# Performance work log

Measured on AMD Instinct MI355X. Metric: run time of the kernel, lower is better.

## Reference

```python
import jax, jax.numpy as jnp
import numpy as np

VERY_NEG = -1e30


def setup_inputs() -> dict:
    key = jax.random.key(0)
    kq, kk, kv, km = jax.random.split(key, 4)
    B, H, S, D = 4, 8, 2048, 64
    Q = jax.random.normal(kq, (B, H, S, D), dtype=jnp.float32)
    K = jax.random.normal(kk, (B, H, S, D), dtype=jnp.float32)
    V = jax.random.normal(kv, (B, H, S, D), dtype=jnp.float32)
    # key-padding mask broadcast over heads and queries: 1 = keep, 0 = masked
    mask = jax.random.randint(km, (B, 1, 1, S), 0, 2, dtype=jnp.int32)
    return {"Q": Q, "K": K, "V": V, "mask": mask}


def reference(Q, K, V, mask):
    d_k = Q.shape[-1]
    scale = jnp.asarray(np.power(d_k, 0.5), dtype=Q.dtype)
    # scores: [B,H,S_q,S_k]
    scores = jnp.einsum("bhqd,bhkd->bhqk", Q, K) / scale
    # QANet exponential_mask: add -1e30 where mask == 0
    masked = scores + (1.0 - mask.astype(scores.dtype)) * VERY_NEG
    attn = jax.nn.softmax(masked, axis=-1)
    out = jnp.einsum("bhqk,bhkd->bhqd", attn, V)
    return out
```

## Files before the change

### kernel.cpp

```cpp
#include <hip/hip_runtime.h>

typedef _Float16 half8_t __attribute__((ext_vector_type(8)));
typedef _Float16 half4_t __attribute__((ext_vector_type(4)));
typedef _Float16 half2_t __attribute__((ext_vector_type(2)));
typedef __fp16 fp16x2 __attribute__((ext_vector_type(2)));
typedef float f32x4 __attribute__((ext_vector_type(4)));

#define S_LEN 2048
#define D_DIM 64
#define SD (S_LEN * D_DIM)
#define NT16 16
#define LDK 72
#define LDO 68
#define THR 4.0f
#define WS_NEED ((size_t)(16 * 1024 * 1024 + 16384))

__global__ __launch_bounds__(256)
void prep_kernel(const float* __restrict__ Kg, const float* __restrict__ Vg,
                 const int* __restrict__ Mg, _Float16* __restrict__ wsK,
                 _Float16* __restrict__ wsV, _Float16* __restrict__ wsKeep) {
  __shared__ float vt[64][68];
  const int blk = blockIdx.x;
  const int t = threadIdx.x;

  if (blk < 1024) {
    const int bh = blk >> 5, kt = blk & 31;
    const float* src = Kg + (size_t)bh * SD + (size_t)kt * 64 * D_DIM;
    char* dst = (char*)wsK + (size_t)blk * 8192;
#pragma unroll
    for (int i = 0; i < 2; ++i) {
      int task = t + 256 * i;
      int row = task >> 3, j = task & 7;
      float4 lo = *(const float4*)(src + row * D_DIM + 8 * j);
      float4 hi = *(const float4*)(src + row * D_DIM + 8 * j + 4);
      fp16x2 p0 = __builtin_amdgcn_cvt_pkrtz(lo.x, lo.y);
      fp16x2 p1 = __builtin_amdgcn_cvt_pkrtz(lo.z, lo.w);
      fp16x2 p2 = __builtin_amdgcn_cvt_pkrtz(hi.x, hi.y);
      fp16x2 p3 = __builtin_amdgcn_cvt_pkrtz(hi.z, hi.w);
      half8_t h;
      h[0] = (_Float16)p0[0]; h[1] = (_Float16)p0[1];
      h[2] = (_Float16)p1[0]; h[3] = (_Float16)p1[1];
      h[4] = (_Float16)p2[0]; h[5] = (_Float16)p2[1];
      h[6] = (_Float16)p3[0]; h[7] = (_Float16)p3[1];
      *(half8_t*)(dst + row * 128 + ((16 * j) ^ ((row & 7) << 4))) = h;
    }
  } else if (blk < 2048) {
    const int vb = blk - 1024;
    const int bh = vb >> 5, kt = vb & 31;
    const float* src = Vg + (size_t)bh * SD + (size_t)kt * 64 * D_DIM;
    const int* msk = Mg + (size_t)(bh >> 3) * S_LEN + kt * 64;
#pragma unroll
    for (int i = 0; i < 4; ++i) {
      int r = (t >> 4) + 16 * i, c4 = t & 15;
      *(float4*)&vt[r][c4 * 4] = *(const float4*)(src + r * D_DIM + c4 * 4);
    }
    __syncthreads();
    char* dst = (char*)wsV + (size_t)vb * 8192;
#pragma unroll
    for (int i = 0; i < 4; ++i) {
      int task = t + 256 * i;
      int drow = task >> 4, j2 = task & 15, k0 = 4 * j2;
      int4 mv = *(const int4*)(msk + k0);
      float a  = vt[k0][drow]     * (float)mv.x;
      float b  = vt[k0 + 1][drow] * (float)mv.y;
      float cc = vt[k0 + 2][drow] * (float)mv.z;
      float d  = vt[k0 + 3][drow] * (float)mv.w;
      fp16x2 h0 = __builtin_amdgcn_cvt_pkrtz(a, b);
      fp16x2 h1 = __builtin_amdgcn_cvt_pkrtz(cc, d);
      half4_t h;
      h[0] = (_Float16)h0[0]; h[1] = (_Float16)h0[1];
      h[2] = (_Float16)h1[0]; h[3] = (_Float16)h1[1];
      *(half4_t*)(dst + drow * 128 + ((8 * j2) ^ ((drow & 15) << 3))) = h;
    }
  } else {
    const int b = blk - 2048;
    const int* src = Mg + (size_t)b * S_LEN + 8 * t;
    int4 m0 = *(const int4*)src;
    int4 m1 = *(const int4*)(src + 4);
    half8_t h;
    h[0] = (_Float16)(float)m0.x; h[1] = (_Float16)(float)m0.y;
    h[2] = (_Float16)(float)m0.z; h[3] = (_Float16)(float)m0.w;
    h[4] = (_Float16)(float)m1.x; h[5] = (_Float16)(float)m1.y;
    h[6] = (_Float16)(float)m1.z; h[7] = (_Float16)(float)m1.w;
    *(half8_t*)(wsKeep + (size_t)b * S_LEN + 8 * t) = h;
  }
}

__global__ __launch_bounds__(256, 2)
void fattn_dma(const float* __restrict__ Qg, const _Float16* __restrict__ wsK,
               const _Float16* __restrict__ wsV,
               const _Float16* __restrict__ wsKeep, float* __restrict__ Og) {
  __shared__ __align__(16) char smem[65536];
  float* Osh = (float*)smem;

  const int t = threadIdx.x;
  const int w = t >> 6;
  const int lane = t & 63;
  const int g = lane >> 4;
  const int c = lane & 15;

  const int bh = blockIdx.x & 31;
  const int qt = blockIdx.x >> 5;
  const int qb = qt * 128;

  const float* Qb = Qg + (size_t)bh * SD;
  float*       Ob = Og + (size_t)bh * SD;
  const _Float16* keepB = wsKeep + (size_t)(bh >> 3) * S_LEN;

  const float qscale = 0.125f * 1.44269504088896340736f;
  half8_t qf[2][2];
#pragma unroll
  for (int h = 0; h < 2; ++h) {
    const float* qp = Qb + (size_t)(qb + 32 * w + 16 * h + c) * D_DIM + 8 * g;
#pragma unroll
    for (int ks = 0; ks < 2; ++ks) {
      float4 lo = *(const float4*)(qp + 32 * ks);
      float4 hi = *(const float4*)(qp + 32 * ks + 4);
      fp16x2 p0 = __builtin_amdgcn_cvt_pkrtz(lo.x * qscale, lo.y * qscale);
      fp16x2 p1 = __builtin_amdgcn_cvt_pkrtz(lo.z * qscale, lo.w * qscale);
      fp16x2 p2 = __builtin_amdgcn_cvt_pkrtz(hi.x * qscale, hi.y * qscale);
      fp16x2 p3 = __builtin_amdgcn_cvt_pkrtz(hi.z * qscale, hi.w * qscale);
      half8_t hh;
      hh[0] = (_Float16)p0[0]; hh[1] = (_Float16)p0[1];
      hh[2] = (_Float16)p1[0]; hh[3] = (_Float16)p1[1];
      hh[4] = (_Float16)p2[0]; hh[5] = (_Float16)p2[1];
      hh[6] = (_Float16)p3[0]; hh[7] = (_Float16)p3[1];
      qf[h][ks] = hh;
    }
  }

  const size_t tbase = (size_t)bh * 32 * 8192;
  auto dma = [&](int buf, int kt) {
    const char* gK = (const char*)wsK + tbase + (size_t)kt * 16384 +
                     w * 4096 + lane * 16;
    const char* gV = (const char*)wsV + tbase + (size_t)kt * 16384 +
                     w * 4096 + lane * 16;
    char* lK = smem + 16384 * buf + w * 4096;
    char* lV = smem + 32768 + 16384 * buf + w * 4096;
#pragma unroll
    for (int i = 0; i < 4; ++i)
      __builtin_amdgcn_global_load_lds((const float*)(gK + 1024 * i),
                                       (float*)(lK + 1024 * i), 16, 0, 0);
#pragma unroll
    for (int i = 0; i < 4; ++i)
      __builtin_amdgcn_global_load_lds((const float*)(gV + 1024 * i),
                                       (float*)(lV + 1024 * i), 16, 0, 0);
  };

  f32x4 acc[2][4];
  f32x4 accl[2];
#pragma unroll
  for (int h = 0; h < 2; ++h) {
#pragma unroll
    for (int j = 0; j < 4; ++j) accl[h][j] = 0.f;
#pragma unroll
    for (int i = 0; i < 4; ++i)
#pragma unroll
      for (int j = 0; j < 4; ++j) acc[h][i][j] = 0.f;
  }
  float mrun[2] = {-1e30f, -1e30f};

  const int kxor = (c & 7) << 4;
  const int vxor = c << 3;

  dma(0, 0);
  __syncthreads();

  for (int kt = 0; kt < NT16; ++kt) {
    const int cur = kt & 1;
    if (kt < NT16 - 1) dma(cur ^ 1, kt + 1);

    const char* Kc = smem + 16384 * cur;
    const char* Vc = smem + 32768 + 16384 * cur;

    half4_t kA[8];
#pragma unroll
    for (int mt = 0; mt < 8; ++mt)
      kA[mt] = *(const half4_t*)(keepB + kt * 128 + 16 * mt + 4 * g);

    f32x4 sT[2][8];
    __builtin_amdgcn_s_setprio(1);
#pragma unroll
    for (int mt = 0; mt < 8; ++mt) {
      const char* Krow = Kc + ((mt & 4) ? 8192 : 0) + (16 * (mt & 3) + c) * 128;
      f32x4 z0, z1;
#pragma unroll
      for (int j = 0; j < 4; ++j) { z0[j] = 0.f; z1[j] = 0.f; }
#pragma unroll
      for (int ks = 0; ks < 2; ++ks) {
        half8_t kf = *(const half8_t*)(Krow + ((ks * 64 + g * 16) ^ kxor));
        z0 = __builtin_amdgcn_mfma_f32_16x16x32_f16(kf, qf[0][ks], z0, 0, 0, 0);
        z1 = __builtin_amdgcn_mfma_f32_16x16x32_f16(kf, qf[1][ks], z1, 0, 0, 0);
      }
      sT[0][mt] = z0;
      sT[1][mt] = z1;
    }
    __builtin_amdgcn_s_setprio(0);

    float tl[2];
#pragma unroll
    for (int h = 0; h < 2; ++h) {
      float tm = -1e30f;
#pragma unroll
      for (int mt = 0; mt < 8; ++mt)
        tm = fmaxf(tm, fmaxf(fmaxf(sT[h][mt][0], sT[h][mt][1]),
                             fmaxf(sT[h][mt][2], sT[h][mt][3])));
      tl[h] = tm;
    }
    int ok0 = __all(tl[0] <= mrun[0] + THR);
    int ok1 = __all(tl[1] <= mrun[1] + THR);
    if (!(ok0 & ok1)) {
#pragma unroll
      for (int h = 0; h < 2; ++h) {
        float tmax = tl[h];
        tmax = fmaxf(tmax, __shfl_xor(tmax, 16));
        tmax = fmaxf(tmax, __shfl_xor(tmax, 32));
        float mnew = fmaxf(mrun[h], tmax);
        float alpha = __builtin_amdgcn_exp2f(mrun[h] - mnew);
        mrun[h] = mnew;
        accl[h][0] *= alpha; accl[h][1] *= alpha;
        accl[h][2] *= alpha; accl[h][3] *= alpha;
#pragma unroll
        for (int mt = 0; mt < 4; ++mt) {
          acc[h][mt][0] *= alpha; acc[h][mt][1] *= alpha;
          acc[h][mt][2] *= alpha; acc[h][mt][3] *= alpha;
        }
      }
    }

    __builtin_amdgcn_s_setprio(1);
#pragma unroll
    for (int mt = 0; mt < 8; ++mt) {
      const char* Vsub = Vc + ((mt & 4) ? 8192 : 0);
      half4_t pf[2];
#pragma unroll
      for (int h = 0; h < 2; ++h) {
        float pv0 = __builtin_amdgcn_exp2f(sT[h][mt][0] - mrun[h]);
        float pv1 = __builtin_amdgcn_exp2f(sT[h][mt][1] - mrun[h]);
        float pv2 = __builtin_amdgcn_exp2f(sT[h][mt][2] - mrun[h]);
        float pv3 = __builtin_amdgcn_exp2f(sT[h][mt][3] - mrun[h]);
        fp16x2 p01 = __builtin_amdgcn_cvt_pkrtz(pv0, pv1);
        fp16x2 p23 = __builtin_amdgcn_cvt_pkrtz(pv2, pv3);
        half4_t ph;
        ph[0] = (_Float16)p01[0]; ph[1] = (_Float16)p01[1];
        ph[2] = (_Float16)p23[0]; ph[3] = (_Float16)p23[1];
        pf[h] = ph;
      }
      half4_t vf[4];
#pragma unroll
      for (int dt = 0; dt < 4; ++dt)
        vf[dt] = *(const half4_t*)(Vsub + (16 * dt + c) * 128 +
                                   ((32 * (mt & 3) + 8 * g) ^ vxor));
      accl[0] = __builtin_amdgcn_mfma_f32_16x16x16f16(kA[mt], pf[0], accl[0], 0, 0, 0);
      accl[1] = __builtin_amdgcn_mfma_f32_16x16x16f16(kA[mt], pf[1], accl[1], 0, 0, 0);
#pragma unroll
      for (int dt = 0; dt < 4; ++dt) {
        acc[0][dt] = __builtin_amdgcn_mfma_f32_16x16x16f16(vf[dt], pf[0],
                                                           acc[0][dt], 0, 0, 0);
        acc[1][dt] = __builtin_amdgcn_mfma_f32_16x16x16f16(vf[dt], pf[1],
                                                           acc[1][dt], 0, 0, 0);
      }
    }
    __builtin_amdgcn_s_setprio(0);

    __syncthreads();
  }

#pragma unroll
  for (int h = 0; h < 2; ++h) {
    float linv = 1.f / accl[h][0];
#pragma unroll
    for (int mt = 0; mt < 4; ++mt)
#pragma unroll
      for (int r = 0; r < 4; ++r)
        Osh[(32 * w + 16 * h + c) * LDO + 16 * mt + 4 * g + r] = acc[h][mt][r] * linv;
  }
  __syncthreads();
  {
    int f8 = t & 7;
#pragma unroll
    for (int i = 0; i < 4; ++i) {
      int q = (t >> 3) + 32 * i;
#pragma unroll
      for (int j = 0; j < 2; ++j) {
        int c4 = f8 + 8 * j;
        f32x4 o = *(f32x4*)(Osh + q * LDO + c4 * 4);
        *(float4*)(Ob + (size_t)(qb + q) * D_DIM + c4 * 4) =
            make_float4(o.x, o.y, o.z, o.w);
      }
    }
  }
}

__global__ __launch_bounds__(256, 2)
void fattn_fb(const float* __restrict__ Qg, const float* __restrict__ Kg,
              const float* __restrict__ Vg, const int* __restrict__ Mg,
              float* __restrict__ Og) {
  __shared__ __align__(16) char smem[45056];
  float* Msh = (float*)(smem + 36864);
  float* Osh = (float*)smem;

  const int t = threadIdx.x;
  const int w = t >> 6;
  const int lane = t & 63;
  const int g = lane >> 4;
  const int c = lane & 15;

  const int bh = blockIdx.x & 31;
  const int qt = blockIdx.x >> 5;
  const int qb = qt * 128;

  const float* Qb = Qg + (size_t)bh * SD;
  const float* Kb = Kg + (size_t)bh * SD;
  const float* Vb = Vg + (size_t)bh * SD;
  const int*   Mb = Mg + (size_t)(bh >> 3) * S_LEN;
  float*       Ob = Og + (size_t)bh * SD;

  {
    int4 m0 = *(const int4*)(Mb + 8 * t);
    int4 m1 = *(const int4*)(Mb + 8 * t + 4);
    float4 f0, f1;
    f0.x = (float)(m0.x - 1) * 1e30f; f0.y = (float)(m0.y - 1) * 1e30f;
    f0.z = (float)(m0.z - 1) * 1e30f; f0.w = (float)(m0.w - 1) * 1e30f;
    f1.x = (float)(m1.x - 1) * 1e30f; f1.y = (float)(m1.y - 1) * 1e30f;
    f1.z = (float)(m1.z - 1) * 1e30f; f1.w = (float)(m1.w - 1) * 1e30f;
    *(float4*)(Msh + 8 * t) = f0;
    *(float4*)(Msh + 8 * t + 4) = f1;
  }

  const float qscale = 0.125f * 1.44269504088896340736f;
  half8_t qf[2][2];
#pragma unroll
  for (int h = 0; h < 2; ++h) {
    const float* qp = Qb + (size_t)(qb + 32 * w + 16 * h + c) * D_DIM + 8 * g;
#pragma unroll
    for (int ks = 0; ks < 2; ++ks) {
      float4 lo = *(const float4*)(qp + 32 * ks);
      float4 hi = *(const float4*)(qp + 32 * ks + 4);
      fp16x2 p0 = __builtin_amdgcn_cvt_pkrtz(lo.x * qscale, lo.y * qscale);
      fp16x2 p1 = __builtin_amdgcn_cvt_pkrtz(lo.z * qscale, lo.w * qscale);
      fp16x2 p2 = __builtin_amdgcn_cvt_pkrtz(hi.x * qscale, hi.y * qscale);
      fp16x2 p3 = __builtin_amdgcn_cvt_pkrtz(hi.z * qscale, hi.w * qscale);
      half8_t hh;
      hh[0] = (_Float16)p0[0]; hh[1] = (_Float16)p0[1];
      hh[2] = (_Float16)p1[0]; hh[3] = (_Float16)p1[1];
      hh[4] = (_Float16)p2[0]; hh[5] = (_Float16)p2[1];
      hh[6] = (_Float16)p3[0]; hh[7] = (_Float16)p3[1];
      qf[h][ks] = hh;
    }
  }

  const int krow0 = t >> 4;
  const int kc4   = t & 15;
  const int vp    = t >> 3;
  const int vkpl  = t & 7;

  float4 kr[4];
  float2 vr[8];
  auto prefetch = [&](int kb2) {
#pragma unroll
    for (int it = 0; it < 4; ++it)
      kr[it] = *(const float4*)(Kb + (size_t)(kb2 + krow0 + 16 * it) * D_DIM + kc4 * 4);
#pragma unroll
    for (int kc = 0; kc < 4; ++kc) {
      const float* vpp = Vb + (size_t)(kb2 + 2 * (vkpl + 8 * kc)) * D_DIM + 2 * vp;
      vr[2 * kc]     = *(const float2*)(vpp);
      vr[2 * kc + 1] = *(const float2*)(vpp + D_DIM);
    }
  };
  auto stage = [&](int buf) {
    _Float16* Kd = (_Float16*)(smem + 9216 * buf);
    _Float16* Vd = (_Float16*)(smem + 18432 + 9216 * buf);
#pragma unroll
    for (int it = 0; it < 4; ++it) {
      fp16x2 a  = __builtin_amdgcn_cvt_pkrtz(kr[it].x, kr[it].y);
      fp16x2 b2 = __builtin_amdgcn_cvt_pkrtz(kr[it].z, kr[it].w);
      half4_t h;
      h[0] = (_Float16)a[0]; h[1] = (_Float16)a[1];
      h[2] = (_Float16)b2[0]; h[3] = (_Float16)b2[1];
      *(half4_t*)(Kd + (krow0 + 16 * it) * LDK + kc4 * 4) = h;
    }
#pragma unroll
    for (int kc = 0; kc < 4; ++kc) {
      int kp = vkpl + 8 * kc;
      fp16x2 h0 = __builtin_amdgcn_cvt_pkrtz(vr[2 * kc].x, vr[2 * kc + 1].x);
      fp16x2 h1 = __builtin_amdgcn_cvt_pkrtz(vr[2 * kc].y, vr[2 * kc + 1].y);
      half2_t g0; g0[0] = (_Float16)h0[0]; g0[1] = (_Float16)h0[1];
      half2_t g1; g1[0] = (_Float16)h1[0]; g1[1] = (_Float16)h1[1];
      *(half2_t*)(Vd + (2 * vp) * LDK + 2 * kp) = g0;
      *(half2_t*)(Vd + (2 * vp + 1) * LDK + 2 * kp) = g1;
    }
  };

  f32x4 acc[2][4];
  f32x4 accl[2];
#pragma unroll
  for (int h = 0; h < 2; ++h) {
#pragma unroll
    for (int j = 0; j < 4; ++j) accl[h][j] = 0.f;
#pragma unroll
    for (int i = 0; i < 4; ++i)
#pragma unroll
      for (int j = 0; j < 4; ++j) acc[h][i][j] = 0.f;
  }
// ... 105 lines not shown
        accl[h] = __builtin_amdgcn_mfma_f32_16x16x16f16(ones4, pf, accl[h], 0, 0, 0);
#pragma unroll
        for (int dt = 0; dt < 4; ++dt)
          acc[h][dt] = __builtin_amdgcn_mfma_f32_16x16x16f16(vf[dt][mt], pf,
                                                             acc[h][dt], 0, 0, 0);
      }
    }
    __builtin_amdgcn_s_setprio(0);

    __syncthreads();
  }

#pragma unroll
  for (int h = 0; h < 2; ++h) {
    float linv = 1.f / accl[h][0];
#pragma unroll
    for (int mt = 0; mt < 4; ++mt)
#pragma unroll
      for (int r = 0; r < 4; ++r)
        Osh[(32 * w + 16 * h + c) * LDO + 16 * mt + 4 * g + r] = acc[h][mt][r] * linv;
  }
  __syncthreads();
  {
    int f8 = t & 7;
#pragma unroll
    for (int i = 0; i < 4; ++i) {
      int q = (t >> 3) + 32 * i;
#pragma unroll
      for (int j = 0; j < 2; ++j) {
        int c4 = f8 + 8 * j;
        f32x4 o = *(f32x4*)(Osh + q * LDO + c4 * 4);
        *(float4*)(Ob + (size_t)(qb + q) * D_DIM + c4 * 4) =
            make_float4(o.x, o.y, o.z, o.w);
      }
    }
  }
}

extern "C" void kernel_launch(void* const* d_in, const int* in_sizes, int n_in,
                              void* d_out, int out_size, void* d_ws, size_t ws_size,
                              hipStream_t stream) {
  (void)in_sizes; (void)n_in; (void)out_size;
  const float* Q = (const float*)d_in[0];
  const float* K = (const float*)d_in[1];
  const float* V = (const float*)d_in[2];
  const int*   M = (const int*)d_in[3];
  float* O = (float*)d_out;

  if (ws_size >= WS_NEED && d_ws != nullptr) {
    _Float16* wsK = (_Float16*)d_ws;
    _Float16* wsV = wsK + (size_t)32 * S_LEN * D_DIM;
    _Float16* wsKeep = (_Float16*)((char*)d_ws + 16 * 1024 * 1024);
    prep_kernel<<<dim3(2052), dim3(256), 0, stream>>>(K, V, M, wsK, wsV, wsKeep);
    fattn_dma<<<dim3(32 * 16), dim3(256), 0, stream>>>(Q, wsK, wsV, wsKeep, O);
  } else {
    fattn_fb<<<dim3(32 * 16), dim3(256), 0, stream>>>(Q, K, V, M, O);
  }
}
```

Baseline: 144.3 us.

## Replace LDS double-buffered attention with register-direct fragment loads and smaller query tiles

The main attention kernel stops staging K and V tiles through LDS with DMA and barriers. Each wave now loads its MFMA fragments straight from global memory into registers, using a two-set ping-pong software pipeline. The prep kernel drops the XOR swizzle and reorders the V layout so that fragments can be read directly. Query tiles shrink from 128 to 64 rows, doubling the grid and raising occupancy to 4 blocks per CU. The cost is that each block rereads the per-head K/V through cache, with more global traffic and more load latency exposed per wave.

```diff
diff --git a/kernel.cpp b/kernel.cpp
--- a/kernel.cpp
+++ b/kernel.cpp
@@ -9,7 +9,6 @@
 #define S_LEN 2048
 #define D_DIM 64
 #define SD (S_LEN * D_DIM)
-#define NT16 16
 #define LDK 72
 #define LDO 68
 #define THR 4.0f
@@ -42,7 +41,7 @@
       h[2] = (_Float16)p1[0]; h[3] = (_Float16)p1[1];
       h[4] = (_Float16)p2[0]; h[5] = (_Float16)p2[1];
       h[6] = (_Float16)p3[0]; h[7] = (_Float16)p3[1];
-      *(half8_t*)(dst + row * 128 + ((16 * j) ^ ((row & 7) << 4))) = h;
+      *(half8_t*)(dst + row * 128 + 16 * j) = h;
     }
   } else if (blk < 2048) {
     const int vb = blk - 1024;
@@ -59,7 +58,8 @@
 #pragma unroll
     for (int i = 0; i < 4; ++i) {
       int task = t + 256 * i;
-      int drow = task >> 4, j2 = task & 15, k0 = 4 * j2;
+      int drow = task >> 4, j2 = task & 15;
+      int k0 = 16 * (2 * (j2 >> 3) + (j2 & 1)) + 4 * ((j2 >> 1) & 3);
       int4 mv = *(const int4*)(msk + k0);
       float a  = vt[k0][drow]     * (float)mv.x;
       float b  = vt[k0 + 1][drow] * (float)mv.y;
@@ -70,7 +70,7 @@
       half4_t h;
       h[0] = (_Float16)h0[0]; h[1] = (_Float16)h0[1];
       h[2] = (_Float16)h1[0]; h[3] = (_Float16)h1[1];
-      *(half4_t*)(dst + drow * 128 + ((8 * j2) ^ ((drow & 15) << 3))) = h;
+      *(half4_t*)(dst + drow * 128 + 8 * j2) = h;
     }
   } else {
     const int b = blk - 2048;
@@ -86,12 +86,11 @@
   }
 }
 
-__global__ __launch_bounds__(256, 2)
-void fattn_dma(const float* __restrict__ Qg, const _Float16* __restrict__ wsK,
+__global__ __launch_bounds__(256, 4)
+void fattn_reg(const float* __restrict__ Qg, const _Float16* __restrict__ wsK,
                const _Float16* __restrict__ wsV,
                const _Float16* __restrict__ wsKeep, float* __restrict__ Og) {
-  __shared__ __align__(16) char smem[65536];
-  float* Osh = (float*)smem;
+  __shared__ float Osh[64 * LDO];
 
   const int t = threadIdx.x;
   const int w = t >> 6;
@@ -101,11 +100,207 @@
 
   const int bh = blockIdx.x & 31;
   const int qt = blockIdx.x >> 5;
-  const int qb = qt * 128;
+  const int qb = qt * 64;
 
   const float* Qb = Qg + (size_t)bh * SD;
   float*       Ob = Og + (size_t)bh * SD;
-  const _Float16* keepB = wsKeep + (size_t)(bh >> 3) * S_LEN;
+
+  const float qscale = 0.125f * 1.44269504088896340736f;
+  half8_t qf0, qf1;
+  {
+    const float* qp = Qb + (size_t)(qb + 16 * w + c) * D_DIM + 8 * g;
+#pragma unroll
+    for (int ks = 0; ks < 2; ++ks) {
+      float4 lo = *(const float4*)(qp + 32 * ks);
+      float4 hi = *(const float4*)(qp + 32 * ks + 4);
+      fp16x2 p0 = __builtin_amdgcn_cvt_pkrtz(lo.x * qscale, lo.y * qscale);
+      fp16x2 p1 = __builtin_amdgcn_cvt_pkrtz(lo.z * qscale, lo.w * qscale);
+      fp16x2 p2 = __builtin_amdgcn_cvt_pkrtz(hi.x * qscale, hi.y * qscale);
+      fp16x2 p3 = __builtin_amdgcn_cvt_pkrtz(hi.z * qscale, hi.w * qscale);
+      half8_t hh;
+      hh[0] = (_Float16)p0[0]; hh[1] = (_Float16)p0[1];
+      hh[2] = (_Float16)p1[0]; hh[3] = (_Float16)p1[1];
+      hh[4] = (_Float16)p2[0]; hh[5] = (_Float16)p2[1];
+      hh[6] = (_Float16)p3[0]; hh[7] = (_Float16)p3[1];
+      if (ks == 0) qf0 = hh; else qf1 = hh;
+    }
+  }
+
+  const char* kB  = (const char*)wsK + (size_t)bh * 262144 + (size_t)c * 128 + g * 16;
+  const char* vB0 = (const char*)wsV + (size_t)bh * 262144 + (size_t)c * 128 + g * 16;
+  const char* vB1 = vB0 + 4096;
+  const _Float16* kpB = wsKeep + (size_t)(bh >> 3) * S_LEN + 4 * g;
+
+  struct FragSet {
+    half8_t kf00, kf01, kf10, kf11;
+    half8_t vf0, vf1, vf2, vf3;
+    half4_t kA0, kA1;
+  };
+
+  auto loadSet = [&](FragSet& S, const char* kp, const char* v0,
+                     const char* v1, const _Float16* kpp, int ho)
+      __attribute__((always_inline)) {
+    S.kf00 = *(const half8_t*)(kp);
+    S.kf01 = *(const half8_t*)(kp + 64);
+    S.kf10 = *(const half8_t*)(kp + 2048);
+    S.kf11 = *(const half8_t*)(kp + 2112);
+    S.vf0 = *(const half8_t*)(v0 + ho);
+    S.vf1 = *(const half8_t*)(v0 + 2048 + ho);
+    S.vf2 = *(const half8_t*)(v1 + ho);
+    S.vf3 = *(const half8_t*)(v1 + 2048 + ho);
+    S.kA0 = *(const half4_t*)(kpp);
+    S.kA1 = *(const half4_t*)(kpp + 16);
+  };
+
+  f32x4 acc0 = {0.f,0.f,0.f,0.f}, acc1 = {0.f,0.f,0.f,0.f};
+  f32x4 acc2 = {0.f,0.f,0.f,0.f}, acc3 = {0.f,0.f,0.f,0.f};
+  f32x4 accl = {0.f,0.f,0.f,0.f};
+  float mrun = -1e30f;
+
+  auto compute = [&](FragSet& S) __attribute__((always_inline)) {
+    __builtin_amdgcn_s_setprio(1);
+    f32x4 s0 = {0.f,0.f,0.f,0.f}, s1 = {0.f,0.f,0.f,0.f};
+    s0 = __builtin_amdgcn_mfma_f32_16x16x32_f16(S.kf00, qf0, s0, 0, 0, 0);
+    s0 = __builtin_amdgcn_mfma_f32_16x16x32_f16(S.kf01, qf1, s0, 0, 0, 0);
+    s1 = __builtin_amdgcn_mfma_f32_16x16x32_f16(S.kf10, qf0, s1, 0, 0, 0);
+    s1 = __builtin_amdgcn_mfma_f32_16x16x32_f16(S.kf11, qf1, s1, 0, 0, 0);
+    __builtin_amdgcn_s_setprio(0);
+
+    float tl = fmaxf(fmaxf(fmaxf(s0[0], s0[1]), fmaxf(s0[2], s0[3])),
+                     fmaxf(fmaxf(s1[0], s1[1]), fmaxf(s1[2], s1[3])));
+    if (!__all(tl <= mrun + THR)) {
+      float tmax = fmaxf(tl, __shfl_xor(tl, 16));
+      tmax = fmaxf(tmax, __shfl_xor(tmax, 32));
+      float mnew = fmaxf(mrun, tmax);
+      float alpha = __builtin_amdgcn_exp2f(mrun - mnew);
+      mrun = mnew;
+#pragma unroll
+      for (int r = 0; r < 4; ++r) {
+        accl[r] *= alpha;
+        acc0[r] *= alpha; acc1[r] *= alpha;
+        acc2[r] *= alpha; acc3[r] *= alpha;
+      }
+    }
+
+    float p00 = __builtin_amdgcn_exp2f(s0[0] - mrun);
+    float p01 = __builtin_amdgcn_exp2f(s0[1] - mrun);
+    float p02 = __builtin_amdgcn_exp2f(s0[2] - mrun);
+    float p03 = __builtin_amdgcn_exp2f(s0[3] - mrun);
+    float p10 = __builtin_amdgcn_exp2f(s1[0] - mrun);
+    float p11 = __builtin_amdgcn_exp2f(s1[1] - mrun);
+    float p12 = __builtin_amdgcn_exp2f(s1[2] - mrun);
+    float p13 = __builtin_amdgcn_exp2f(s1[3] - mrun);
+    fp16x2 a0 = __builtin_amdgcn_cvt_pkrtz(p00, p01);
+    fp16x2 a1 = __builtin_amdgcn_cvt_pkrtz(p02, p03);
+    fp16x2 b0 = __builtin_amdgcn_cvt_pkrtz(p10, p11);
+    fp16x2 b1 = __builtin_amdgcn_cvt_pkrtz(p12, p13);
+    half4_t pf0, pf1;
+    pf0[0] = (_Float16)a0[0]; pf0[1] = (_Float16)a0[1];
+    pf0[2] = (_Float16)a1[0]; pf0[3] = (_Float16)a1[1];
+    pf1[0] = (_Float16)b0[0]; pf1[1] = (_Float16)b0[1];
+    pf1[2] = (_Float16)b1[0]; pf1[3] = (_Float16)b1[1];
+
+    __builtin_amdgcn_s_setprio(1);
+    accl = __builtin_amdgcn_mfma_f32_16x16x16f16(S.kA0, pf0, accl, 0, 0, 0);
+    accl = __builtin_amdgcn_mfma_f32_16x16x16f16(S.kA1, pf1, accl, 0, 0, 0);
+    half4_t v;
+    v = __builtin_shufflevector(S.vf0, S.vf0, 0, 1, 2, 3);
+    acc0 = __builtin_amdgcn_mfma_f32_16x16x16f16(v, pf0, acc0, 0, 0, 0);
+    v = __builtin_shufflevector(S.vf0, S.vf0, 4, 5, 6, 7);
+    acc0 = __builtin_amdgcn_mfma_f32_16x16x16f16(v, pf1, acc0, 0, 0, 0);
+    v = __builtin_shufflevector(S.vf1, S.vf1, 0, 1, 2, 3);
+    acc1 = __builtin_amdgcn_mfma_f32_16x16x16f16(v, pf0, acc1, 0, 0, 0);
+    v = __builtin_shufflevector(S.vf1, S.vf1, 4, 5, 6, 7);
+    acc1 = __builtin_amdgcn_mfma_f32_16x16x16f16(v, pf1, acc1, 0, 0, 0);
+    v = __builtin_shufflevector(S.vf2, S.vf2, 0, 1, 2, 3);
+    acc2 = __builtin_amdgcn_mfma_f32_16x16x16f16(v, pf0, acc2, 0, 0, 0);
+    v = __builtin_shufflevector(S.vf2, S.vf2, 4, 5, 6, 7);
+    acc2 = __builtin_amdgcn_mfma_f32_16x16x16f16(v, pf1, acc2, 0, 0, 0);
+    v = __builtin_shufflevector(S.vf3, S.vf3, 0, 1, 2, 3);
+    acc3 = __builtin_amdgcn_mfma_f32_16x16x16f16(v, pf0, acc3, 0, 0, 0);
+    v = __builtin_shufflevector(S.vf3, S.vf3, 4, 5, 6, 7);
+    acc3 = __builtin_amdgcn_mfma_f32_16x16x16f16(v, pf1, acc3, 0, 0, 0);
+    __builtin_amdgcn_s_setprio(0);
+  };
+
+  FragSet A, B;
+  loadSet(A, kB, vB0, vB1, kpB, 0);
+  kB += 4096; kpB += 32;
+  for (int tt = 0; tt < 62; tt += 2) {
+    loadSet(B, kB, vB0, vB1, kpB, 64);
+    kB += 4096; kpB += 32; vB0 += 8192; vB1 += 8192;
+    compute(A);
+    loadSet(A, kB, vB0, vB1, kpB, 0);
+    kB += 4096; kpB += 32;
+    compute(B);
+  }
+  loadSet(B, kB, vB0, vB1, kpB, 64);
+  compute(A);
+  compute(B);
+
+  {
+    float linv = 1.f / accl[0];
+    int row = (16 * w + c) * LDO + 4 * g;
+#pragma unroll
+    for (int r = 0; r < 4; ++r) {
+      Osh[row + 0  + r] = acc0[r] * linv;
+      Osh[row + 16 + r] = acc1[r] * linv;
+      Osh[row + 32 + r] = acc2[r] * linv;
+      Osh[row + 48 + r] = acc3[r] * linv;
+    }
+  }
+  __syncthreads();
+  {
+    int f8 = t & 7;
+#pragma unroll
+    for (int i = 0; i < 2; ++i) {
+      int q = (t >> 3) + 32 * i;
+#pragma unroll
+      for (int j = 0; j < 2; ++j) {
+        int c4 = f8 + 8 * j;
+        f32x4 o = *(f32x4*)(Osh + q * LDO + c4 * 4);
+        *(float4*)(Ob + (size_t)(qb + q) * D_DIM + c4 * 4) =
+            make_float4(o.x, o.y, o.z, o.w);
+      }
+    }
+  }
+}
+
+__global__ __launch_bounds__(256, 2)
+void fattn_fb(const float* __restrict__ Qg, const float* __restrict__ Kg,
+              const float* __restrict__ Vg, const int* __restrict__ Mg,
+              float* __restrict__ Og) {
+  __shared__ __align__(16) char smem[45056];
+  float* Msh = (float*)(smem + 36864);
+  float* Osh = (float*)smem;
+
+  const int t = threadIdx.x;
+  const int w = t >> 6;
+  const int lane = t & 63;
+  const int g = lane >> 4;
+  const int c = lane & 15;
+
+  const int bh = blockIdx.x & 31;
+  const int qt = blockIdx.x >> 5;
+  const int qb = qt * 128;
+
+  const float* Qb = Qg + (size_t)bh * SD;
+  const float* Kb = Kg + (size_t)bh * SD;
+  const float* Vb = Vg + (size_t)bh * SD;
+  const int*   Mb = Mg + (size_t)(bh >> 3) * S_LEN;
+  float*       Ob = Og + (size_t)bh * SD;
+
+  {
+    int4 m0 = *(const int4*)(Mb + 8 * t);
+    int4 m1 = *(const int4*)(Mb + 8 * t + 4);
+    float4 f0, f1;
+    f0.x = (float)(m0.x - 1) * 1e30f; f0.y = (float)(m0.y - 1) * 1e30f;
+    f0.z = (float)(m0.z - 1) * 1e30f; f0.w = (float)(m0.w - 1) * 1e30f;
+    f1.x = (float)(m1.x - 1) * 1e30f; f1.y = (float)(m1.y - 1) * 1e30f;
+    f1.z = (float)(m1.z - 1) * 1e30f; f1.w = (float)(m1.w - 1) * 1e30f;
+    *(float4*)(Msh + 8 * t) = f0;
+    *(float4*)(Msh + 8 * t + 4) = f1;
+  }
 
   const float qscale = 0.125f * 1.44269504088896340736f;
   half8_t qf[2][2];
@@ -129,227 +324,6 @@
     }
   }
 
-  const size_t tbase = (size_t)bh * 32 * 8192;
-  auto dma = [&](int buf, int kt) {
-    const char* gK = (const char*)wsK + tbase + (size_t)kt * 16384 +
-                     w * 4096 + lane * 16;
-    const char* gV = (const char*)wsV + tbase + (size_t)kt * 16384 +
-                     w * 4096 + lane * 16;
-    char* lK = smem + 16384 * buf + w * 4096;
-    char* lV = smem + 32768 + 16384 * buf + w * 4096;
-#pragma unroll
-    for (int i = 0; i < 4; ++i)
-      __builtin_amdgcn_global_load_lds((const float*)(gK + 1024 * i),
-                                       (float*)(lK + 1024 * i), 16, 0, 0);
-#pragma unroll
-    for (int i = 0; i < 4; ++i)
-      __builtin_amdgcn_global_load_lds((const float*)(gV + 1024 * i),
-                                       (float*)(lV + 1024 * i), 16, 0, 0);
-  };
-
-  f32x4 acc[2][4];
-  f32x4 accl[2];
-#pragma unroll
-  for (int h = 0; h < 2; ++h) {
-#pragma unroll
-    for (int j = 0; j < 4; ++j) accl[h][j] = 0.f;
-#pragma unroll
-    for (int i = 0; i < 4; ++i)
-#pragma unroll
-      for (int j = 0; j < 4; ++j) acc[h][i][j] = 0.f;
-  }
-  float mrun[2] = {-1e30f, -1e30f};
-
-  const int kxor = (c & 7) << 4;
-  const int vxor = c << 3;
-
-  dma(0, 0);
-  __syncthreads();
-
-  for (int kt = 0; kt < NT16; ++kt) {
-    const int cur = kt & 1;
-    if (kt < NT16 - 1) dma(cur ^ 1, kt + 1);
-
-    const char* Kc = smem + 16384 * cur;
-    const char* Vc = smem + 32768 + 16384 * cur;
-
-    half4_t kA[8];
-#pragma unroll
-    for (int mt = 0; mt < 8; ++mt)
-      kA[mt] = *(const half4_t*)(keepB + kt * 128 + 16 * mt + 4 * g);
-
-    f32x4 sT[2][8];
-    __builtin_amdgcn_s_setprio(1);
-#pragma unroll
-    for (int mt = 0; mt < 8; ++mt) {
-      const char* Krow = Kc + ((mt & 4) ? 8192 : 0) + (16 * (mt & 3) + c) * 128;
-      f32x4 z0, z1;
-#pragma unroll
-      for (int j = 0; j < 4; ++j) { z0[j] = 0.f; z1[j] = 0.f; }
-#pragma unroll
-      for (int ks = 0; ks < 2; ++ks) {
-        half8_t kf = *(const half8_t*)(Krow + ((ks * 64 + g * 16) ^ kxor));
-        z0 = __builtin_amdgcn_mfma_f32_16x16x32_f16(kf, qf[0][ks], z0, 0, 0, 0);
-        z1 = __builtin_amdgcn_mfma_f32_16x16x32_f16(kf, qf[1][ks], z1, 0, 0, 0);
-      }
-      sT[0][mt] = z0;
-      sT[1][mt] = z1;
-    }
-    __builtin_amdgcn_s_setprio(0);
-
-    float tl[2];
-#pragma unroll
-    for (int h = 0; h < 2; ++h) {
-      float tm = -1e30f;
-#pragma unroll
-      for (int mt = 0; mt < 8; ++mt)
-        tm = fmaxf(tm, fmaxf(fmaxf(sT[h][mt][0], sT[h][mt][1]),
-                             fmaxf(sT[h][mt][2], sT[h][mt][3])));
-      tl[h] = tm;
-    }
-    int ok0 = __all(tl[0] <= mrun[0] + THR);
-    int ok1 = __all(tl[1] <= mrun[1] + THR);
-    if (!(ok0 & ok1)) {
-#pragma unroll
-      for (int h = 0; h < 2; ++h) {
-        float tmax = tl[h];
-        tmax = fmaxf(tmax, __shfl_xor(tmax, 16));
-        tmax = fmaxf(tmax, __shfl_xor(tmax, 32));
-        float mnew = fmaxf(mrun[h], tmax);
-        float alpha = __builtin_amdgcn_exp2f(mrun[h] - mnew);
-        mrun[h] = mnew;
-        accl[h][0] *= alpha; accl[h][1] *= alpha;
-        accl[h][2] *= alpha; accl[h][3] *= alpha;
-#pragma unroll
-        for (int mt = 0; mt < 4; ++mt) {
-          acc[h][mt][0] *= alpha; acc[h][mt][1] *= alpha;
-          acc[h][mt][2] *= alpha; acc[h][mt][3] *= alpha;
-        }
-      }
-    }
-
-    __builtin_amdgcn_s_setprio(1);
-#pragma unroll
-    for (int mt = 0; mt < 8; ++mt) {
-      const char* Vsub = Vc + ((mt & 4) ? 8192 : 0);
-      half4_t pf[2];
-#pragma unroll
-      for (int h = 0; h < 2; ++h) {
-        float pv0 = __builtin_amdgcn_exp2f(sT[h][mt][0] - mrun[h]);
-        float pv1 = __builtin_amdgcn_exp2f(sT[h][mt][1] - mrun[h]);
-        float pv2 = __builtin_amdgcn_exp2f(sT[h][mt][2] - mrun[h]);
-        float pv3 = __builtin_amdgcn_exp2f(sT[h][mt][3] - mrun[h]);
-        fp16x2 p01 = __builtin_amdgcn_cvt_pkrtz(pv0, pv1);
-        fp16x2 p23 = __builtin_amdgcn_cvt_pkrtz(pv2, pv3);
-        half4_t ph;
-        ph[0] = (_Float16)p01[0]; ph[1] = (_Float16)p01[1];
-        ph[2] = (_Float16)p23[0]; ph[3] = (_Float16)p23[1];
-        pf[h] = ph;
-      }
-      half4_t vf[4];
-#pragma unroll
-      for (int dt = 0; dt < 4; ++dt)
-        vf[dt] = *(const half4_t*)(Vsub + (16 * dt + c) * 128 +
-                                   ((32 * (mt & 3) + 8 * g) ^ vxor));
-      accl[0] = __builtin_amdgcn_mfma_f32_16x16x16f16(kA[mt], pf[0], accl[0], 0, 0, 0);
-      accl[1] = __builtin_amdgcn_mfma_f32_16x16x16f16(kA[mt], pf[1], accl[1], 0, 0, 0);
-#pragma unroll
-      for (int dt = 0; dt < 4; ++dt) {
-        acc[0][dt] = __builtin_amdgcn_mfma_f32_16x16x16f16(vf[dt], pf[0],
-                                                           acc[0][dt], 0, 0, 0);
-        acc[1][dt] = __builtin_amdgcn_mfma_f32_16x16x16f16(vf[dt], pf[1],
-                                                           acc[1][dt], 0, 0, 0);
-      }
-    }
-    __builtin_amdgcn_s_setprio(0);
-
-    __syncthreads();
-  }
-
-#pragma unroll
-  for (int h = 0; h < 2; ++h) {
-    float linv = 1.f / accl[h][0];
-#pragma unroll
-    for (int mt = 0; mt < 4; ++mt)
-#pragma unroll
-      for (int r = 0; r < 4; ++r)
-        Osh[(32 * w + 16 * h + c) * LDO + 16 * mt + 4 * g + r] = acc[h][mt][r] * linv;
-  }
-  __syncthreads();
-  {
-    int f8 = t & 7;
-#pragma unroll
-    for (int i = 0; i < 4; ++i) {
-      int q = (t >> 3) + 32 * i;
-#pragma unroll
-      for (int j = 0; j < 2; ++j) {
-        int c4 = f8 + 8 * j;
-        f32x4 o = *(f32x4*)(Osh + q * LDO + c4 * 4);
-        *(float4*)(Ob + (size_t)(qb + q) * D_DIM + c4 * 4) =
-            make_float4(o.x, o.y, o.z, o.w);
-      }
-    }
-  }
-}
-
-__global__ __launch_bounds__(256, 2)
-void fattn_fb(const float* __restrict__ Qg, const float* __restrict__ Kg,
-              const float* __restrict__ Vg, const int* __restrict__ Mg,
-              float* __restrict__ Og) {
-  __shared__ __align__(16) char smem[45056];
-  float* Msh = (float*)(smem + 36864);
-  float* Osh = (float*)smem;
-
-  const int t = threadIdx.x;
-  const int w = t >> 6;
-  const int lane = t & 63;
-  const int g = lane >> 4;
-  const int c = lane & 15;
-
-  const int bh = blockIdx.x & 31;
-  const int qt = blockIdx.x >> 5;
-  const int qb = qt * 128;
-
-  const float* Qb = Qg + (size_t)bh * SD;
-  const float* Kb = Kg + (size_t)bh * SD;
-  const float* Vb = Vg + (size_t)bh * SD;
-  const int*   Mb = Mg + (size_t)(bh >> 3) * S_LEN;
-  float*       Ob = Og + (size_t)bh * SD;
-
-  {
-    int4 m0 = *(const int4*)(Mb + 8 * t);
-    int4 m1 = *(const int4*)(Mb + 8 * t + 4);
-    float4 f0, f1;
-    f0.x = (float)(m0.x - 1) * 1e30f; f0.y = (float)(m0.y - 1) * 1e30f;
-    f0.z = (float)(m0.z - 1) * 1e30f; f0.w = (float)(m0.w - 1) * 1e30f;
-    f1.x = (float)(m1.x - 1) * 1e30f; f1.y = (float)(m1.y - 1) * 1e30f;
-    f1.z = (float)(m1.z - 1) * 1e30f; f1.w = (float)(m1.w - 1) * 1e30f;
-    *(float4*)(Msh + 8 * t) = f0;
-    *(float4*)(Msh + 8 * t + 4) = f1;
-  }
-
-  const float qscale = 0.125f * 1.44269504088896340736f;
-  half8_t qf[2][2];
-#pragma unroll
-  for (int h = 0; h < 2; ++h) {
-    const float* qp = Qb + (size_t)(qb + 32 * w + 16 * h + c) * D_DIM + 8 * g;
-#pragma unroll
-    for (int ks = 0; ks < 2; ++ks) {
-      float4 lo = *(const float4*)(qp + 32 * ks);
-      float4 hi = *(const float4*)(qp + 32 * ks + 4);
-      fp16x2 p0 = __builtin_amdgcn_cvt_pkrtz(lo.x * qscale, lo.y * qscale);
-      fp16x2 p1 = __builtin_amdgcn_cvt_pkrtz(lo.z * qscale, lo.w * qscale);
-      fp16x2 p2 = __builtin_amdgcn_cvt_pkrtz(hi.x * qscale, hi.y * qscale);
-      fp16x2 p3 = __builtin_amdgcn_cvt_pkrtz(hi.z * qscale, hi.w * qscale);
-      half8_t hh;
-      hh[0] = (_Float16)p0[0]; hh[1] = (_Float16)p0[1];
-      hh[2] = (_Float16)p1[0]; hh[3] = (_Float16)p1[1];
-      hh[4] = (_Float16)p2[0]; hh[5] = (_Float16)p2[1];
-      hh[6] = (_Float16)p3[0]; hh[7] = (_Float16)p3[1];
-      qf[h][ks] = hh;
-    }
-  }
-
   const int krow0 = t >> 4;
   const int kc4   = t & 15;
   const int vp    = t >> 3;
@@ -561,7 +535,7 @@
     _Float16* wsV = wsK + (size_t)32 * S_LEN * D_DIM;
     _Float16* wsKeep = (_Float16*)((char*)d_ws + 16 * 1024 * 1024);
     prep_kernel<<<dim3(2052), dim3(256), 0, stream>>>(K, V, M, wsK, wsV, wsKeep);
-    fattn_dma<<<dim3(32 * 16), dim3(256), 0, stream>>>(Q, wsK, wsV, wsKeep, O);
+    fattn_reg<<<dim3(32 * 32), dim3(256), 0, stream>>>(Q, wsK, wsV, wsKeep, O);
   } else {
     fattn_fb<<<dim3(32 * 16), dim3(256), 0, stream>>>(Q, K, V, M, O);
   }
```

Result: slower. 334.4 us (+131.6%).

## Halve attention query tile to 64 rows and double grid for occupancy

Applied to the files above, without the earlier changes.

The main attention kernel now handles 64 query rows per block (16 per wave) instead of 128, with 64-key tiles and half the LDS (32KB). The grid doubles to 1024 blocks and launch bounds allow 4 blocks per CU. V fragments are loaded for the whole tile ahead of the softmax. The goal is higher occupancy and better latency hiding across CUs. The cost is that every K/V tile is loaded from memory twice as often, with less reuse per load and more loop iterations and barriers.

```diff
diff --git a/kernel.cpp b/kernel.cpp
--- a/kernel.cpp
+++ b/kernel.cpp
@@ -9,7 +9,6 @@
 #define S_LEN 2048
 #define D_DIM 64
 #define SD (S_LEN * D_DIM)
-#define NT16 16
 #define LDK 72
 #define LDO 68
 #define THR 4.0f
@@ -86,11 +85,11 @@
   }
 }
 
-__global__ __launch_bounds__(256, 2)
+__global__ __launch_bounds__(256, 4)
 void fattn_dma(const float* __restrict__ Qg, const _Float16* __restrict__ wsK,
                const _Float16* __restrict__ wsV,
                const _Float16* __restrict__ wsKeep, float* __restrict__ Og) {
-  __shared__ __align__(16) char smem[65536];
+  __shared__ __align__(16) char smem[32768];
   float* Osh = (float*)smem;
 
   const int t = threadIdx.x;
@@ -101,11 +100,204 @@
 
   const int bh = blockIdx.x & 31;
   const int qt = blockIdx.x >> 5;
-  const int qb = qt * 128;
+  const int qb = qt * 64;
 
   const float* Qb = Qg + (size_t)bh * SD;
   float*       Ob = Og + (size_t)bh * SD;
   const _Float16* keepB = wsKeep + (size_t)(bh >> 3) * S_LEN;
+
+  const float qscale = 0.125f * 1.44269504088896340736f;
+  half8_t qf[2];
+  {
+    const float* qp = Qb + (size_t)(qb + 16 * w + c) * D_DIM + 8 * g;
+#pragma unroll
+    for (int ks = 0; ks < 2; ++ks) {
+      float4 lo = *(const float4*)(qp + 32 * ks);
+      float4 hi = *(const float4*)(qp + 32 * ks + 4);
+      fp16x2 p0 = __builtin_amdgcn_cvt_pkrtz(lo.x * qscale, lo.y * qscale);
+      fp16x2 p1 = __builtin_amdgcn_cvt_pkrtz(lo.z * qscale, lo.w * qscale);
+      fp16x2 p2 = __builtin_amdgcn_cvt_pkrtz(hi.x * qscale, hi.y * qscale);
+      fp16x2 p3 = __builtin_amdgcn_cvt_pkrtz(hi.z * qscale, hi.w * qscale);
+      half8_t hh;
+      hh[0] = (_Float16)p0[0]; hh[1] = (_Float16)p0[1];
+      hh[2] = (_Float16)p1[0]; hh[3] = (_Float16)p1[1];
+      hh[4] = (_Float16)p2[0]; hh[5] = (_Float16)p2[1];
+      hh[6] = (_Float16)p3[0]; hh[7] = (_Float16)p3[1];
+      qf[ks] = hh;
+    }
+  }
+
+  const size_t tbase = (size_t)bh * 262144;
+  auto dma = [&](int buf, int kt) {
+    const char* gK = (const char*)wsK + tbase + (size_t)kt * 8192 +
+                     w * 2048 + lane * 16;
+    const char* gV = (const char*)wsV + tbase + (size_t)kt * 8192 +
+                     w * 2048 + lane * 16;
+    char* lK = smem + 8192 * buf + w * 2048;
+    char* lV = smem + 16384 + 8192 * buf + w * 2048;
+    __builtin_amdgcn_global_load_lds((const float*)gK, (float*)lK, 16, 0, 0);
+    __builtin_amdgcn_global_load_lds((const float*)(gK + 1024),
+                                     (float*)(lK + 1024), 16, 0, 0);
+    __builtin_amdgcn_global_load_lds((const float*)gV, (float*)lV, 16, 0, 0);
+    __builtin_amdgcn_global_load_lds((const float*)(gV + 1024),
+                                     (float*)(lV + 1024), 16, 0, 0);
+  };
+
+  f32x4 acc[4];
+  f32x4 accl;
+#pragma unroll
+  for (int j = 0; j < 4; ++j) {
+    accl[j] = 0.f;
+#pragma unroll
+    for (int i = 0; i < 4; ++i) acc[i][j] = 0.f;
+  }
+  float mrun = -1e30f;
+
+  const int kxor = (c & 7) << 4;
+  const int vxor = c << 3;
+
+  dma(0, 0);
+  __syncthreads();
+
+  for (int kt = 0; kt < 32; ++kt) {
+    const int cur = kt & 1;
+    if (kt < 31) dma(cur ^ 1, kt + 1);
+
+    const char* Kc = smem + 8192 * cur;
+    const char* Vc = smem + 16384 + 8192 * cur;
+
+    half4_t kA[4];
+#pragma unroll
+    for (int mt = 0; mt < 4; ++mt)
+      kA[mt] = *(const half4_t*)(keepB + kt * 64 + 16 * mt + 4 * g);
+
+    f32x4 sT[4];
+    __builtin_amdgcn_s_setprio(1);
+#pragma unroll
+    for (int mt = 0; mt < 4; ++mt) {
+      const char* Krow = Kc + (16 * mt + c) * 128;
+      f32x4 z;
+#pragma unroll
+      for (int j = 0; j < 4; ++j) z[j] = 0.f;
+#pragma unroll
+      for (int ks = 0; ks < 2; ++ks) {
+        half8_t kf = *(const half8_t*)(Krow + ((ks * 64 + g * 16) ^ kxor));
+        z = __builtin_amdgcn_mfma_f32_16x16x32_f16(kf, qf[ks], z, 0, 0, 0);
+      }
+      sT[mt] = z;
+    }
+    __builtin_amdgcn_s_setprio(0);
+
+    half4_t vf[4][4];
+#pragma unroll
+    for (int dt = 0; dt < 4; ++dt)
+#pragma unroll
+      for (int mtk = 0; mtk < 4; ++mtk)
+        vf[dt][mtk] = *(const half4_t*)(Vc + (16 * dt + c) * 128 +
+                                        ((32 * mtk + 8 * g) ^ vxor));
+
+    float tl = -1e30f;
+#pragma unroll
+    for (int mt = 0; mt < 4; ++mt)
+      tl = fmaxf(tl, fmaxf(fmaxf(sT[mt][0], sT[mt][1]),
+                           fmaxf(sT[mt][2], sT[mt][3])));
+    if (!__all(tl <= mrun + THR)) {
+      float tmax = fmaxf(tl, __shfl_xor(tl, 16));
+      tmax = fmaxf(tmax, __shfl_xor(tmax, 32));
+      float mnew = fmaxf(mrun, tmax);
+      float alpha = __builtin_amdgcn_exp2f(mrun - mnew);
+      mrun = mnew;
+#pragma unroll
+      for (int j = 0; j < 4; ++j) {
+        accl[j] *= alpha;
+#pragma unroll
+        for (int i = 0; i < 4; ++i) acc[i][j] *= alpha;
+      }
+    }
+
+    __builtin_amdgcn_s_setprio(1);
+#pragma unroll
+    for (int mt = 0; mt < 4; ++mt) {
+      float pv0 = __builtin_amdgcn_exp2f(sT[mt][0] - mrun);
+      float pv1 = __builtin_amdgcn_exp2f(sT[mt][1] - mrun);
+      float pv2 = __builtin_amdgcn_exp2f(sT[mt][2] - mrun);
+      float pv3 = __builtin_amdgcn_exp2f(sT[mt][3] - mrun);
+      fp16x2 p01 = __builtin_amdgcn_cvt_pkrtz(pv0, pv1);
+      fp16x2 p23 = __builtin_amdgcn_cvt_pkrtz(pv2, pv3);
+      half4_t pf;
+      pf[0] = (_Float16)p01[0]; pf[1] = (_Float16)p01[1];
+      pf[2] = (_Float16)p23[0]; pf[3] = (_Float16)p23[1];
+      accl = __builtin_amdgcn_mfma_f32_16x16x16f16(kA[mt], pf, accl, 0, 0, 0);
+#pragma unroll
+      for (int dt = 0; dt < 4; ++dt)
+        acc[dt] = __builtin_amdgcn_mfma_f32_16x16x16f16(vf[dt][mt], pf,
+                                                        acc[dt], 0, 0, 0);
+    }
+    __builtin_amdgcn_s_setprio(0);
+
+    __syncthreads();
+  }
+
+  {
+    float linv = 1.f / accl[0];
+#pragma unroll
+    for (int mt = 0; mt < 4; ++mt)
+#pragma unroll
+      for (int r = 0; r < 4; ++r)
+        Osh[(16 * w + c) * LDO + 16 * mt + 4 * g + r] = acc[mt][r] * linv;
+  }
+  __syncthreads();
+  {
+    int f8 = t & 7;
+#pragma unroll
+    for (int i = 0; i < 2; ++i) {
+      int q = (t >> 3) + 32 * i;
+#pragma unroll
+      for (int j = 0; j < 2; ++j) {
+        int c4 = f8 + 8 * j;
+        f32x4 o = *(f32x4*)(Osh + q * LDO + c4 * 4);
+        *(float4*)(Ob + (size_t)(qb + q) * D_DIM + c4 * 4) =
+            make_float4(o.x, o.y, o.z, o.w);
+      }
+    }
+  }
+}
+
+__global__ __launch_bounds__(256, 2)
+void fattn_fb(const float* __restrict__ Qg, const float* __restrict__ Kg,
+              const float* __restrict__ Vg, const int* __restrict__ Mg,
+              float* __restrict__ Og) {
+  __shared__ __align__(16) char smem[45056];
+  float* Msh = (float*)(smem + 36864);
+  float* Osh = (float*)smem;
+
+  const int t = threadIdx.x;
+  const int w = t >> 6;
+  const int lane = t & 63;
+  const int g = lane >> 4;
+  const int c = lane & 15;
+
+  const int bh = blockIdx.x & 31;
+  const int qt = blockIdx.x >> 5;
+  const int qb = qt * 128;
+
+  const float* Qb = Qg + (size_t)bh * SD;
+  const float* Kb = Kg + (size_t)bh * SD;
+  const float* Vb = Vg + (size_t)bh * SD;
+  const int*   Mb = Mg + (size_t)(bh >> 3) * S_LEN;
+  float*       Ob = Og + (size_t)bh * SD;
+
+  {
+    int4 m0 = *(const int4*)(Mb + 8 * t);
+    int4 m1 = *(const int4*)(Mb + 8 * t + 4);
+    float4 f0, f1;
+    f0.x = (float)(m0.x - 1) * 1e30f; f0.y = (float)(m0.y - 1) * 1e30f;
+    f0.z = (float)(m0.z - 1) * 1e30f; f0.w = (float)(m0.w - 1) * 1e30f;
+    f1.x = (float)(m1.x - 1) * 1e30f; f1.y = (float)(m1.y - 1) * 1e30f;
+    f1.z = (float)(m1.z - 1) * 1e30f; f1.w = (float)(m1.w - 1) * 1e30f;
+    *(float4*)(Msh + 8 * t) = f0;
+    *(float4*)(Msh + 8 * t + 4) = f1;
+  }
 
   const float qscale = 0.125f * 1.44269504088896340736f;
   half8_t qf[2][2];
@@ -129,227 +321,6 @@
     }
   }
 
-  const size_t tbase = (size_t)bh * 32 * 8192;
-  auto dma = [&](int buf, int kt) {
-    const char* gK = (const char*)wsK + tbase + (size_t)kt * 16384 +
-                     w * 4096 + lane * 16;
-    const char* gV = (const char*)wsV + tbase + (size_t)kt * 16384 +
-                     w * 4096 + lane * 16;
-    char* lK = smem + 16384 * buf + w * 4096;
-    char* lV = smem + 32768 + 16384 * buf + w * 4096;
-#pragma unroll
-    for (int i = 0; i < 4; ++i)
-      __builtin_amdgcn_global_load_lds((const float*)(gK + 1024 * i),
-                                       (float*)(lK + 1024 * i), 16, 0, 0);
-#pragma unroll
-    for (int i = 0; i < 4; ++i)
-      __builtin_amdgcn_global_load_lds((const float*)(gV + 1024 * i),
-                                       (float*)(lV + 1024 * i), 16, 0, 0);
-  };
-
-  f32x4 acc[2][4];
-  f32x4 accl[2];
-#pragma unroll
-  for (int h = 0; h < 2; ++h) {
-#pragma unroll
-    for (int j = 0; j < 4; ++j) accl[h][j] = 0.f;
-#pragma unroll
-    for (int i = 0; i < 4; ++i)
-#pragma unroll
-      for (int j = 0; j < 4; ++j) acc[h][i][j] = 0.f;
-  }
-  float mrun[2] = {-1e30f, -1e30f};
-
-  const int kxor = (c & 7) << 4;
-  const int vxor = c << 3;
-
-  dma(0, 0);
-  __syncthreads();
-
-  for (int kt = 0; kt < NT16; ++kt) {
-    const int cur = kt & 1;
-    if (kt < NT16 - 1) dma(cur ^ 1, kt + 1);
-
-    const char* Kc = smem + 16384 * cur;
-    const char* Vc = smem + 32768 + 16384 * cur;
-
-    half4_t kA[8];
-#pragma unroll
-    for (int mt = 0; mt < 8; ++mt)
-      kA[mt] = *(const half4_t*)(keepB + kt * 128 + 16 * mt + 4 * g);
-
-    f32x4 sT[2][8];
-    __builtin_amdgcn_s_setprio(1);
-#pragma unroll
-    for (int mt = 0; mt < 8; ++mt) {
-      const char* Krow = Kc + ((mt & 4) ? 8192 : 0) + (16 * (mt & 3) + c) * 128;
-      f32x4 z0, z1;
-#pragma unroll
-      for (int j = 0; j < 4; ++j) { z0[j] = 0.f; z1[j] = 0.f; }
-#pragma unroll
-      for (int ks = 0; ks < 2; ++ks) {
-        half8_t kf = *(const half8_t*)(Krow + ((ks * 64 + g * 16) ^ kxor));
-        z0 = __builtin_amdgcn_mfma_f32_16x16x32_f16(kf, qf[0][ks], z0, 0, 0, 0);
-        z1 = __builtin_amdgcn_mfma_f32_16x16x32_f16(kf, qf[1][ks], z1, 0, 0, 0);
-      }
-      sT[0][mt] = z0;
-      sT[1][mt] = z1;
-    }
-    __builtin_amdgcn_s_setprio(0);
-
-    float tl[2];
-#pragma unroll
-    for (int h = 0; h < 2; ++h) {
-      float tm = -1e30f;
-#pragma unroll
-      for (int mt = 0; mt < 8; ++mt)
-        tm = fmaxf(tm, fmaxf(fmaxf(sT[h][mt][0], sT[h][mt][1]),
-                             fmaxf(sT[h][mt][2], sT[h][mt][3])));
-      tl[h] = tm;
-    }
-    int ok0 = __all(tl[0] <= mrun[0] + THR);
-    int ok1 = __all(tl[1] <= mrun[1] + THR);
-    if (!(ok0 & ok1)) {
-#pragma unroll
-      for (int h = 0; h < 2; ++h) {
-        float tmax = tl[h];
-        tmax = fmaxf(tmax, __shfl_xor(tmax, 16));
-        tmax = fmaxf(tmax, __shfl_xor(tmax, 32));
-        float mnew = fmaxf(mrun[h], tmax);
-        float alpha = __builtin_amdgcn_exp2f(mrun[h] - mnew);
-        mrun[h] = mnew;
-        accl[h][0] *= alpha; accl[h][1] *= alpha;
-        accl[h][2] *= alpha; accl[h][3] *= alpha;
-#pragma unroll
-        for (int mt = 0; mt < 4; ++mt) {
-          acc[h][mt][0] *= alpha; acc[h][mt][1] *= alpha;
-          acc[h][mt][2] *= alpha; acc[h][mt][3] *= alpha;
-        }
-      }
-    }
-
-    __builtin_amdgcn_s_setprio(1);
-#pragma unroll
-    for (int mt = 0; mt < 8; ++mt) {
-      const char* Vsub = Vc + ((mt & 4) ? 8192 : 0);
-      half4_t pf[2];
-#pragma unroll
-      for (int h = 0; h < 2; ++h) {
-        float pv0 = __builtin_amdgcn_exp2f(sT[h][mt][0] - mrun[h]);
-        float pv1 = __builtin_amdgcn_exp2f(sT[h][mt][1] - mrun[h]);
-        float pv2 = __builtin_amdgcn_exp2f(sT[h][mt][2] - mrun[h]);
-        float pv3 = __builtin_amdgcn_exp2f(sT[h][mt][3] - mrun[h]);
-        fp16x2 p01 = __builtin_amdgcn_cvt_pkrtz(pv0, pv1);
-        fp16x2 p23 = __builtin_amdgcn_cvt_pkrtz(pv2, pv3);
-        half4_t ph;
-        ph[0] = (_Float16)p01[0]; ph[1] = (_Float16)p01[1];
-        ph[2] = (_Float16)p23[0]; ph[3] = (_Float16)p23[1];
-        pf[h] = ph;
-      }
-      half4_t vf[4];
-#pragma unroll
-      for (int dt = 0; dt < 4; ++dt)
-        vf[dt] = *(const half4_t*)(Vsub + (16 * dt + c) * 128 +
-                                   ((32 * (mt & 3) + 8 * g) ^ vxor));
-      accl[0] = __builtin_amdgcn_mfma_f32_16x16x16f16(kA[mt], pf[0], accl[0], 0, 0, 0);
-      accl[1] = __builtin_amdgcn_mfma_f32_16x16x16f16(kA[mt], pf[1], accl[1], 0, 0, 0);
-#pragma unroll
-      for (int dt = 0; dt < 4; ++dt) {
-        acc[0][dt] = __builtin_amdgcn_mfma_f32_16x16x16f16(vf[dt], pf[0],
-                                                           acc[0][dt], 0, 0, 0);
-        acc[1][dt] = __builtin_amdgcn_mfma_f32_16x16x16f16(vf[dt], pf[1],
-                                                           acc[1][dt], 0, 0, 0);
-      }
-    }
-    __builtin_amdgcn_s_setprio(0);
-
-    __syncthreads();
-  }
-
-#pragma unroll
-  for (int h = 0; h < 2; ++h) {
-    float linv = 1.f / accl[h][0];
-#pragma unroll
-    for (int mt = 0; mt < 4; ++mt)
-#pragma unroll
-      for (int r = 0; r < 4; ++r)
-        Osh[(32 * w + 16 * h + c) * LDO + 16 * mt + 4 * g + r] = acc[h][mt][r] * linv;
-  }
-  __syncthreads();
-  {
-    int f8 = t & 7;
-#pragma unroll
-    for (int i = 0; i < 4; ++i) {
-      int q = (t >> 3) + 32 * i;
-#pragma unroll
-      for (int j = 0; j < 2; ++j) {
-        int c4 = f8 + 8 * j;
-        f32x4 o = *(f32x4*)(Osh + q * LDO + c4 * 4);
-        *(float4*)(Ob + (size_t)(qb + q) * D_DIM + c4 * 4) =
-            make_float4(o.x, o.y, o.z, o.w);
-      }
-    }
-  }
-}
-
-__global__ __launch_bounds__(256, 2)
-void fattn_fb(const float* __restrict__ Qg, const float* __restrict__ Kg,
-              const float* __restrict__ Vg, const int* __restrict__ Mg,
-              float* __restrict__ Og) {
-  __shared__ __align__(16) char smem[45056];
-  float* Msh = (float*)(smem + 36864);
-  float* Osh = (float*)smem;
-
-  const int t = threadIdx.x;
-  const int w = t >> 6;
-  const int lane = t & 63;
-  const int g = lane >> 4;
-  const int c = lane & 15;
-
-  const int bh = blockIdx.x & 31;
-  const int qt = blockIdx.x >> 5;
-  const int qb = qt * 128;
-
-  const float* Qb = Qg + (size_t)bh * SD;
-  const float* Kb = Kg + (size_t)bh * SD;
-  const float* Vb = Vg + (size_t)bh * SD;
-  const int*   Mb = Mg + (size_t)(bh >> 3) * S_LEN;
-  float*       Ob = Og + (size_t)bh * SD;
-
-  {
-    int4 m0 = *(const int4*)(Mb + 8 * t);
-    int4 m1 = *(const int4*)(Mb + 8 * t + 4);
-    float4 f0, f1;
-    f0.x = (float)(m0.x - 1) * 1e30f; f0.y = (float)(m0.y - 1) * 1e30f;
-    f0.z = (float)(m0.z - 1) * 1e30f; f0.w = (float)(m0.w - 1) * 1e30f;
-    f1.x = (float)(m1.x - 1) * 1e30f; f1.y = (float)(m1.y - 1) * 1e30f;
-    f1.z = (float)(m1.z - 1) * 1e30f; f1.w = (float)(m1.w - 1) * 1e30f;
-    *(float4*)(Msh + 8 * t) = f0;
-    *(float4*)(Msh + 8 * t + 4) = f1;
-  }
-
-  const float qscale = 0.125f * 1.44269504088896340736f;
-  half8_t qf[2][2];
-#pragma unroll
-  for (int h = 0; h < 2; ++h) {
-    const float* qp = Qb + (size_t)(qb + 32 * w + 16 * h + c) * D_DIM + 8 * g;
-#pragma unroll
-    for (int ks = 0; ks < 2; ++ks) {
-      float4 lo = *(const float4*)(qp + 32 * ks);
-      float4 hi = *(const float4*)(qp + 32 * ks + 4);
-      fp16x2 p0 = __builtin_amdgcn_cvt_pkrtz(lo.x * qscale, lo.y * qscale);
-      fp16x2 p1 = __builtin_amdgcn_cvt_pkrtz(lo.z * qscale, lo.w * qscale);
-      fp16x2 p2 = __builtin_amdgcn_cvt_pkrtz(hi.x * qscale, hi.y * qscale);
-      fp16x2 p3 = __builtin_amdgcn_cvt_pkrtz(hi.z * qscale, hi.w * qscale);
-      half8_t hh;
-      hh[0] = (_Float16)p0[0]; hh[1] = (_Float16)p0[1];
-      hh[2] = (_Float16)p1[0]; hh[3] = (_Float16)p1[1];
-      hh[4] = (_Float16)p2[0]; hh[5] = (_Float16)p2[1];
-      hh[6] = (_Float16)p3[0]; hh[7] = (_Float16)p3[1];
-      qf[h][ks] = hh;
-    }
-  }
-
   const int krow0 = t >> 4;
   const int kc4   = t & 15;
   const int vp    = t >> 3;
@@ -561,7 +532,7 @@
     _Float16* wsV = wsK + (size_t)32 * S_LEN * D_DIM;
     _Float16* wsKeep = (_Float16*)((char*)d_ws + 16 * 1024 * 1024);
     prep_kernel<<<dim3(2052), dim3(256), 0, stream>>>(K, V, M, wsK, wsV, wsKeep);
-    fattn_dma<<<dim3(32 * 16), dim3(256), 0, stream>>>(Q, wsK, wsV, wsKeep, O);
+    fattn_dma<<<dim3(32 * 32), dim3(256), 0, stream>>>(Q, wsK, wsV, wsKeep, O);
   } else {
     fattn_fb<<<dim3(32 * 16), dim3(256), 0, stream>>>(Q, K, V, M, O);
   }
```

After: 147.6 us. 1.02x slower.
